# Kernel optimization log

Measured on AMD Instinct MI355X. Metric: run time of the kernel, lower is better.

## Reference

```python
import jax, jax.numpy as jnp
import numpy as np
import math

B, N, D = 4, 2048, 512
H, DH = 8, 128
INNER = H * DH


def setup_inputs() -> dict:
    key = jax.random.key(0)
    k1, k2, k3, k4 = jax.random.split(key, 4)
    x = jax.random.normal(k1, (B, N, D), dtype=jnp.float32)
    Wg = jax.random.normal(k2, (D, INNER), dtype=jnp.float32) * (1.0 / math.sqrt(D))
    Wout = jax.random.normal(k3, (INNER, D), dtype=jnp.float32) * (1.0 / math.sqrt(INNER))
    sigma = jax.random.uniform(k4, (1, H, 1, 1), dtype=jnp.float32, minval=0.5, maxval=2.5)
    return {"x": x, "Wg": Wg, "Wout": Wout, "sigma": sigma}


def reference(x, Wg, Wout, sigma):
    b, n, d = x.shape
    h, dh = H, DH
    # value projection: [b,n,d] @ [d, h*dh] -> [b,h,n,dh]
    v = (x @ Wg).reshape(b, n, h, dh).transpose(0, 2, 1, 3)
    # fixed Gaussian positional mask, shared across batch: build once per head
    pos = jnp.arange(1, n + 1, dtype=jnp.float32)
    diffs = jnp.abs(pos[:, None] - pos[None, :])  # [n, n]
    sig = sigma.reshape(h, 1, 1)  # [h,1,1]
    inv_norm = 1.0 / (jnp.sqrt(2.0 * jnp.float32(math.pi)) * sig)
    gauss = inv_norm * jnp.exp(-(diffs[None] ** 2) / (2.0 * sig ** 2))  # [h,n,n]
    corr = gauss / gauss.sum(-1, keepdims=True)  # row-normalized [h,n,n]
    # attention: broadcast mask over batch
    attn = jnp.einsum('hnm,bhmd->bhnd', corr, v)
    out = attn.transpose(0, 2, 1, 3).reshape(b, n, h * dh)
    return out @ Wout  # dropout p=0.0 -> identity
```

## Files before the change

kernel.cpp:

```cpp
#include <hip/hip_runtime.h>
#include <hip/hip_bf16.h>
#include <math.h>

#define B_ 4
#define N_ 2048
#define D_ 512
#define H_ 8
#define DH_ 128
#define INNER_ 1024
#define W_ 32
#define M_ (B_ * N_)

typedef __attribute__((ext_vector_type(8))) short short8;
typedef __attribute__((ext_vector_type(4))) float floatx4;

typedef const __attribute__((address_space(1))) char* gcp;
typedef __attribute__((address_space(3))) char* lcp;

__device__ __forceinline__ unsigned f_to_bf16bits(float f) {
    union { float f; unsigned u; } c; c.f = f;
    return (c.u + 0x7fffu + ((c.u >> 16) & 1u)) >> 16;
}
__device__ __forceinline__ float bf16s_to_f(unsigned short s) {
    union { unsigned u; float f; } c; c.u = ((unsigned)s) << 16; return c.f;
}

#define VST 136

__global__ __launch_bounds__(256, 4) void g1_blur(
    const __hip_bfloat16* __restrict__ x_bf,
    const __hip_bfloat16* __restrict__ Wg_t,
    const float* __restrict__ sigma,
    const float* __restrict__ winv_g,
    __hip_bfloat16* __restrict__ attn)
{
    __shared__ char smem[35328];
    __hip_bfloat16* Asm = (__hip_bfloat16*)smem;
    __hip_bfloat16* Bsm = (__hip_bfloat16*)(smem + 16384);

    const int tid  = threadIdx.x;
    const int lane = tid & 63;
    const int w    = tid >> 6;
    const int wm   = w >> 1;
    const int wn   = w & 1;
    const int quad = lane >> 4;
    const int cl   = lane & 15;

    const int L    = blockIdx.x + 128 * blockIdx.y;
    const int xcd  = L & 7;
    const int idx  = L >> 3;
    const int bm   = xcd * 16 + (idx & 15);
    const int h    = idx >> 4;
    const int n0   = bm * 64;
    const int nb0  = n0 & (N_ - 1);

    floatx4 acc[4][4];
    #pragma unroll
    for (int i = 0; i < 4; ++i)
        #pragma unroll
        for (int j = 0; j < 4; ++j) acc[i][j] = (floatx4){0.f, 0.f, 0.f, 0.f};

    const char* Ab = (const char*)x_bf;
    const char* Bb = (const char*)(Wg_t + (size_t)(h * DH_) * D_);

    for (int k0 = 0; k0 < D_; k0 += 64) {
        #pragma unroll
        for (int it = 0; it < 4; ++it) {
            int o = it * 4096 + tid * 16;
            int r = o >> 7;
            int s = (o >> 4) & 7;
            int c = s ^ (r & 7);
            int gr = n0 - W_ + r;
            gr = gr < 0 ? 0 : (gr > M_ - 1 ? M_ - 1 : gr);
            __builtin_amdgcn_global_load_lds(
                (gcp)(Ab + (size_t)gr * 1024 + k0 * 2 + c * 16), (lcp)(smem + o), 16, 0, 0);
            __builtin_amdgcn_global_load_lds(
                (gcp)(Bb + (size_t)r * 1024 + k0 * 2 + c * 16), (lcp)(smem + 16384 + o), 16, 0, 0);
        }
        __syncthreads();

        const short* As = (const short*)Asm;
        const short* Bs = (const short*)Bsm;
        #pragma unroll
        for (int kk = 0; kk < 2; ++kk) {
            short8 af[4], bf[4];
            int ch = kk * 4 + quad;
            #pragma unroll
            for (int t = 0; t < 4; ++t) {
                int ra = wm * 64 + t * 16 + cl;
                int rb = wn * 64 + t * 16 + cl;
                af[t] = *(const short8*)(As + ra * 64 + ((ch ^ (ra & 7)) * 8));
                bf[t] = *(const short8*)(Bs + rb * 64 + ((ch ^ (rb & 7)) * 8));
            }
            #pragma unroll
            for (int i = 0; i < 4; ++i)
                #pragma unroll
                for (int j = 0; j < 4; ++j)
                    acc[i][j] = __builtin_amdgcn_mfma_f32_16x16x32_bf16(
                        af[i], bf[j], acc[i][j], 0, 0, 0);
        }
        __syncthreads();
    }

    unsigned short* vsT   = (unsigned short*)smem;
    unsigned short* wtabS = (unsigned short*)(smem + 34816);

    #pragma unroll
    for (int i = 0; i < 4; ++i) {
        #pragma unroll
        for (int j = 0; j < 4; ++j) {
            int ch   = wn * 64 + j * 16 + cl;
            int row0 = wm * 64 + i * 16 + quad * 4;
            unsigned p01 = 0u, p23 = 0u;
            #pragma unroll
            for (int rr = 0; rr < 4; ++rr) {
                int vb = nb0 - W_ + row0 + rr;
                unsigned bits = (vb >= 0 && vb < N_) ? f_to_bf16bits(acc[i][j][rr]) : 0u;
                if (rr < 2) p01 |= bits << (rr * 16);
                else        p23 |= bits << ((rr - 2) * 16);
            }
            unsigned* dst = (unsigned*)(vsT + ch * VST + row0);
            dst[0] = p01; dst[1] = p23;
        }
    }
    if (tid <= 2 * W_) {
        float sig = sigma[h];
        float d = (float)(tid - W_);
        wtabS[tid] = (unsigned short)f_to_bf16bits(__expf(-d * d / (2.0f * sig * sig)));
    }
    __syncthreads();

    short afr[2][3][8];
    #pragma unroll
    for (int mi = 0; mi < 2; ++mi) {
        int row = wm * 32 + mi * 16 + cl;
        #pragma unroll
        for (int t = 0; t < 3; ++t) {
            int lb = (wm + t) * 32 + quad * 8 - row;
            #pragma unroll
            for (int j = 0; j < 8; ++j) {
                int l = lb + j;
                afr[mi][t][j] = (l >= 0 && l <= 2 * W_) ? (short)wtabS[l] : (short)0;
            }
        }
    }

    floatx4 oacc[2][4];
    #pragma unroll
    for (int mi = 0; mi < 2; ++mi)
        #pragma unroll
        for (int ni = 0; ni < 4; ++ni) oacc[mi][ni] = (floatx4){0.f, 0.f, 0.f, 0.f};

    #pragma unroll
    for (int t = 0; t < 3; ++t) {
        int k4 = wm + t;
        short8 bfr[4];
        #pragma unroll
        for (int ni = 0; ni < 4; ++ni) {
            int ch = wn * 64 + ni * 16 + cl;
            bfr[ni] = *(const short8*)((const short*)vsT + ch * VST + k4 * 32 + quad * 8);
        }
        #pragma unroll
        for (int mi = 0; mi < 2; ++mi)
            #pragma unroll
            for (int ni = 0; ni < 4; ++ni)
                oacc[mi][ni] = __builtin_amdgcn_mfma_f32_16x16x32_bf16(
                    *(short8*)afr[mi][t], bfr[ni], oacc[mi][ni], 0, 0, 0);
    }

    float wv[2][4];
    #pragma unroll
    for (int mi = 0; mi < 2; ++mi)
        #pragma unroll
        for (int r = 0; r < 4; ++r)
            wv[mi][r] = winv_g[h * N_ + nb0 + wm * 32 + mi * 16 + quad * 4 + r];

    #pragma unroll
    for (int mi = 0; mi < 2; ++mi) {
        #pragma unroll
        for (int ni = 0; ni < 4; ++ni) {
            int ch = wn * 64 + ni * 16 + cl;
            #pragma unroll
            for (int r = 0; r < 4; ++r) {
                int orow = wm * 32 + mi * 16 + quad * 4 + r;
                attn[(size_t)(n0 + orow) * INNER_ + h * DH_ + ch] =
                    __float2bfloat16(oacc[mi][ni][r] * wv[mi][r]);
            }
        }
    }
}

__global__ __launch_bounds__(256, 3) void gemm2_dbuf(
    const __hip_bfloat16* __restrict__ A,
    const __hip_bfloat16* __restrict__ Bt,
    float* __restrict__ C)
{
    __shared__ char smem[49152];

    const int bid  = blockIdx.x;
    const int xcd  = bid & 7;
    const int idx  = bid >> 3;
    const int bm   = xcd * 16 + (idx & 15);
    const int bn   = idx >> 4;

    const int tid  = threadIdx.x;
    const int lane = tid & 63;
    const int w    = tid >> 6;
    const int wm   = w >> 1;
    const int wn   = w & 1;
    const int kh   = lane >> 4;
    const int ml   = lane & 15;

    floatx4 acc[2][4];
    #pragma unroll
    for (int i = 0; i < 2; ++i)
        #pragma unroll
        for (int j = 0; j < 4; ++j) acc[i][j] = (floatx4){0.f, 0.f, 0.f, 0.f};

    const char* Ab = (const char*)(A + (size_t)(bm * 64) * INNER_);
    const char* Bb = (const char*)(Bt + (size_t)(bn * 128) * INNER_);

    auto issue = [&](int buf, int k0) {
        #pragma unroll
        for (int it = 0; it < 2; ++it) {
            int o = it * 4096 + tid * 16;
            int r = o >> 7;
            int c = ((o >> 4) & 7) ^ (r & 7);
            __builtin_amdgcn_global_load_lds(
                (gcp)(Ab + (size_t)r * 2048 + k0 * 2 + c * 16),
                (lcp)(smem + buf * 24576 + o), 16, 0, 0);
        }
        #pragma unroll
        for (int it = 0; it < 4; ++it) {
            int o = it * 4096 + tid * 16;
            int r = o >> 7;
            int c = ((o >> 4) & 7) ^ (r & 7);
            __builtin_amdgcn_global_load_lds(
                (gcp)(Bb + (size_t)r * 2048 + k0 * 2 + c * 16),
                (lcp)(smem + buf * 24576 + 8192 + o), 16, 0, 0);
        }
    };
    auto consume = [&](int buf) {
        const short* As = (const short*)(smem + buf * 24576);
        const short* Bs = (const short*)(smem + buf * 24576 + 8192);
        short8 af[2][2], bf[4][2];
        #pragma unroll
        for (int t = 0; t < 2; ++t) {
            int ra = wm * 32 + t * 16 + ml;
            #pragma unroll
            for (int kk = 0; kk < 2; ++kk) {
                int ch = kk * 4 + kh;
                af[t][kk] = *(const short8*)(As + ra * 64 + ((ch ^ (ra & 7)) * 8));
            }
        }
        #pragma unroll
        for (int ni = 0; ni < 4; ++ni) {
            int rb = wn * 64 + ni * 16 + ml;
            #pragma unroll
            for (int kk = 0; kk < 2; ++kk) {
                int ch = kk * 4 + kh;
                bf[ni][kk] = *(const short8*)(Bs + rb * 64 + ((ch ^ (rb & 7)) * 8));
            }
        }
        #pragma unroll
        for (int kk = 0; kk < 2; ++kk)
            #pragma unroll
            for (int i = 0; i < 2; ++i)
                #pragma unroll
                for (int j = 0; j < 4; ++j)
                    acc[i][j] = __builtin_amdgcn_mfma_f32_16x16x32_bf16(
                        af[i][kk], bf[j][kk], acc[i][j], 0, 0, 0);
    };

    const int nk = INNER_ >> 6;
    issue(0, 0);
    for (int kt = 0; kt < nk; kt += 2) {
        __syncthreads();
        if (kt + 1 < nk) issue(1, (kt + 1) << 6);
        consume(0);
        __syncthreads();
        if (kt + 2 < nk) issue(0, (kt + 2) << 6);
        consume(1);
    }
    __syncthreads();

    float* Cs = (float*)smem;
    const int rq = lane >> 4;
    const int cl = lane & 15;
    #pragma unroll
    for (int i = 0; i < 2; ++i)
        #pragma unroll
        for (int j = 0; j < 4; ++j)
            #pragma unroll
            for (int r = 0; r < 4; ++r)
                Cs[(wm * 32 + i * 16 + rq * 4 + r) * 128 + wn * 64 + j * 16 + cl] = acc[i][j][r];
    __syncthreads();

    #pragma unroll
    for (int p = 0; p < 8; ++p) {
        int idx2 = p * 256 + tid;
        int rr = idx2 >> 5;
        int cc = (idx2 & 31) * 4;
        float4 vv = *(const float4*)(Cs + rr * 128 + cc);
        *(float4*)(C + (size_t)(bm * 64 + rr) * D_ + bn * 128 + cc) = vv;
    }
}

__device__ __forceinline__ void transpose32(
    const float* __restrict__ src, __hip_bfloat16* __restrict__ dst,
    int R, int Cn, int rt, int ct, int tid)
{
    __shared__ float t[32][33];
    int c0 = ct * 32, r0 = rt * 32;
    int lx = tid & 31, ly = tid >> 5;
    #pragma unroll
    for (int i = 0; i < 32; i += 8)
        t[ly + i][lx] = src[(size_t)(r0 + ly + i) * Cn + c0 + lx];
    __syncthreads();
    #pragma unroll
    for (int i = 0; i < 32; i += 8)
        dst[(size_t)(c0 + ly + i) * R + r0 + lx] = __float2bfloat16(t[lx][ly + i]);
}

__global__ __launch_bounds__(256) void prep(
    const float* __restrict__ x, const float* __restrict__ Wg,
    const float* __restrict__ Wout, const float* __restrict__ sigma,
    __hip_bfloat16* __restrict__ x_bf, __hip_bfloat16* __restrict__ Wg_t,
    __hip_bfloat16* __restrict__ Wout_t, float* __restrict__ winv_g)
{
    const int bid = blockIdx.x;
    const int tid = threadIdx.x;
    if (bid < 2048) {
        int i = bid * 256 + tid;
        const float4* s = (const float4*)x + (size_t)i * 2;
        float4 a = s[0], b = s[1];
        __hip_bfloat16 o[8] = {
            __float2bfloat16(a.x), __float2bfloat16(a.y), __float2bfloat16(a.z), __float2bfloat16(a.w),
            __float2bfloat16(b.x), __float2bfloat16(b.y), __float2bfloat16(b.z), __float2bfloat16(b.w)};
        *(short8*)(x_bf + (size_t)i * 8) = *(short8*)o;
    } else if (bid < 2560) {
        int id2 = bid - 2048;
        transpose32(Wg, Wg_t, D_, INNER_, id2 >> 5, id2 & 31, tid);
    } else if (bid < 3072) {
        int id2 = bid - 2560;
        transpose32(Wout, Wout_t, INNER_, D_, id2 >> 4, id2 & 15, tid);
    } else {
        int idx = (bid - 3072) * 256 + tid;
        int hh = idx >> 11;
        int n  = idx & (N_ - 1);
        float sig = sigma[hh];
        float ws = 0.f;
        for (int l = 0; l <= 2 * W_; ++l) {
            int vb = n + l - W_;
            if (vb >= 0 && vb < N_) {
                float d = (float)(l - W_);
                ws += bf16s_to_f((unsigned short)f_to_bf16bits(
                    __expf(-d * d / (2.0f * sig * sig))));
            }
        }
        winv_g[idx] = 1.0f / ws;
    }
}

extern "C" void kernel_launch(void* const* d_in, const int* in_sizes, int n_in,
                              void* d_out, int out_size, void* d_ws, size_t ws_size,
                              hipStream_t stream) {
    const float* x     = (const float*)d_in[0];
    const float* Wg    = (const float*)d_in[1];
    const float* Wout  = (const float*)d_in[2];
    const float* sigma = (const float*)d_in[3];
    float* out = (float*)d_out;

    char* ws = (char*)d_ws;
    __hip_bfloat16* x_bf   = (__hip_bfloat16*)ws;
    __hip_bfloat16* Wg_t   = (__hip_bfloat16*)(ws + (((size_t)8)  << 20));
    __hip_bfloat16* Wout_t = (__hip_bfloat16*)(ws + (((size_t)9)  << 20));
    __hip_bfloat16* attn   = (__hip_bfloat16*)(ws + (((size_t)10) << 20));
    float*          winv_g = (float*)(ws + (((size_t)26) << 20));

    prep<<<dim3(3136), dim3(256), 0, stream>>>(x, Wg, Wout, sigma,
                                               x_bf, Wg_t, Wout_t, winv_g);

    g1_blur<<<dim3(M_ / 64, H_), dim3(256), 0, stream>>>(x_bf, Wg_t, sigma, winv_g, attn);

    gemm2_dbuf<<<dim3(512), dim3(256), 0, stream>>>(attn, Wout_t, out);
}
```

Before: 118.4 us.

## Enlarge fused projection-blur tile to 128 rows to cut halo recompute

The fused value-projection plus Gaussian blur kernel now covers 128 output rows per block instead of 64, using 512 threads and a 192-row projection tile. This lowers the share of redundant halo rows recomputed in the first GEMM from 2x to 1.5x. The cost is more LDS and fewer, larger blocks (512 in total), which reduces occupancy and wave-level parallelism. The load of the normalization weights is also hoisted ahead of the blur stage.

```diff
diff --git a/kernel.cpp b/kernel.cpp
--- a/kernel.cpp
+++ b/kernel.cpp
@@ -25,18 +25,18 @@
     union { unsigned u; float f; } c; c.u = ((unsigned)s) << 16; return c.f;
 }
 
-#define VST 136
-
-__global__ __launch_bounds__(256, 4) void g1_blur(
+#define VST2 200
+#define AROWS 192
+#define BOFF 24576
+
+__global__ __launch_bounds__(512, 2) void g1_blur(
     const __hip_bfloat16* __restrict__ x_bf,
     const __hip_bfloat16* __restrict__ Wg_t,
     const float* __restrict__ sigma,
     const float* __restrict__ winv_g,
     __hip_bfloat16* __restrict__ attn)
 {
-    __shared__ char smem[35328];
-    __hip_bfloat16* Asm = (__hip_bfloat16*)smem;
-    __hip_bfloat16* Bsm = (__hip_bfloat16*)(smem + 16384);
+    __shared__ char smem[51456];
 
     const int tid  = threadIdx.x;
     const int lane = tid & 63;
@@ -46,17 +46,17 @@
     const int quad = lane >> 4;
     const int cl   = lane & 15;
 
-    const int L    = blockIdx.x + 128 * blockIdx.y;
+    const int L    = blockIdx.x + 64 * blockIdx.y;
     const int xcd  = L & 7;
     const int idx  = L >> 3;
-    const int bm   = xcd * 16 + (idx & 15);
-    const int h    = idx >> 4;
-    const int n0   = bm * 64;
+    const int bm   = xcd * 8 + (idx & 7);
+    const int h    = idx >> 3;
+    const int n0   = bm * 128;
     const int nb0  = n0 & (N_ - 1);
 
-    floatx4 acc[4][4];
-    #pragma unroll
-    for (int i = 0; i < 4; ++i)
+    floatx4 acc[3][4];
+    #pragma unroll
+    for (int i = 0; i < 3; ++i)
         #pragma unroll
         for (int j = 0; j < 4; ++j) acc[i][j] = (floatx4){0.f, 0.f, 0.f, 0.f};
 
@@ -65,35 +65,43 @@
 
     for (int k0 = 0; k0 < D_; k0 += 64) {
         #pragma unroll
-        for (int it = 0; it < 4; ++it) {
-            int o = it * 4096 + tid * 16;
+        for (int it = 0; it < 3; ++it) {
+            int o = it * 8192 + tid * 16;
             int r = o >> 7;
-            int s = (o >> 4) & 7;
-            int c = s ^ (r & 7);
+            int c = ((o >> 4) & 7) ^ (r & 7);
             int gr = n0 - W_ + r;
             gr = gr < 0 ? 0 : (gr > M_ - 1 ? M_ - 1 : gr);
             __builtin_amdgcn_global_load_lds(
                 (gcp)(Ab + (size_t)gr * 1024 + k0 * 2 + c * 16), (lcp)(smem + o), 16, 0, 0);
+        }
+        #pragma unroll
+        for (int it = 0; it < 2; ++it) {
+            int o = it * 8192 + tid * 16;
+            int r = o >> 7;
+            int c = ((o >> 4) & 7) ^ (r & 7);
             __builtin_amdgcn_global_load_lds(
-                (gcp)(Bb + (size_t)r * 1024 + k0 * 2 + c * 16), (lcp)(smem + 16384 + o), 16, 0, 0);
+                (gcp)(Bb + (size_t)r * 1024 + k0 * 2 + c * 16), (lcp)(smem + BOFF + o), 16, 0, 0);
         }
         __syncthreads();
 
-        const short* As = (const short*)Asm;
-        const short* Bs = (const short*)Bsm;
+        const short* As = (const short*)smem;
+        const short* Bs = (const short*)(smem + BOFF);
         #pragma unroll
         for (int kk = 0; kk < 2; ++kk) {
-            short8 af[4], bf[4];
+            short8 af[3], bf[4];
             int ch = kk * 4 + quad;
             #pragma unroll
+            for (int t = 0; t < 3; ++t) {
+                int ra = wm * 48 + t * 16 + cl;
+                af[t] = *(const short8*)(As + ra * 64 + ((ch ^ (ra & 7)) * 8));
+            }
+            #pragma unroll
             for (int t = 0; t < 4; ++t) {
-                int ra = wm * 64 + t * 16 + cl;
                 int rb = wn * 64 + t * 16 + cl;
-                af[t] = *(const short8*)(As + ra * 64 + ((ch ^ (ra & 7)) * 8));
                 bf[t] = *(const short8*)(Bs + rb * 64 + ((ch ^ (rb & 7)) * 8));
             }
             #pragma unroll
-            for (int i = 0; i < 4; ++i)
+            for (int i = 0; i < 3; ++i)
                 #pragma unroll
                 for (int j = 0; j < 4; ++j)
                     acc[i][j] = __builtin_amdgcn_mfma_f32_16x16x32_bf16(
@@ -102,15 +110,22 @@
         __syncthreads();
     }
 
+    float wv[2][4];
+    #pragma unroll
+    for (int mi = 0; mi < 2; ++mi)
+        #pragma unroll
+        for (int r = 0; r < 4; ++r)
+            wv[mi][r] = winv_g[h * N_ + nb0 + wm * 32 + mi * 16 + quad * 4 + r];
+
     unsigned short* vsT   = (unsigned short*)smem;
-    unsigned short* wtabS = (unsigned short*)(smem + 34816);
-
-    #pragma unroll
-    for (int i = 0; i < 4; ++i) {
+    unsigned short* wtabS = (unsigned short*)(smem + 51200);
+
+    #pragma unroll
+    for (int i = 0; i < 3; ++i) {
         #pragma unroll
         for (int j = 0; j < 4; ++j) {
             int ch   = wn * 64 + j * 16 + cl;
-            int row0 = wm * 64 + i * 16 + quad * 4;
+            int row0 = wm * 48 + i * 16 + quad * 4;
             unsigned p01 = 0u, p23 = 0u;
             #pragma unroll
             for (int rr = 0; rr < 4; ++rr) {
@@ -119,7 +134,7 @@
                 if (rr < 2) p01 |= bits << (rr * 16);
                 else        p23 |= bits << ((rr - 2) * 16);
             }
-            unsigned* dst = (unsigned*)(vsT + ch * VST + row0);
+            unsigned* dst = (unsigned*)(vsT + ch * VST2 + row0);
             dst[0] = p01; dst[1] = p23;
         }
     }
@@ -153,12 +168,12 @@
 
     #pragma unroll
     for (int t = 0; t < 3; ++t) {
-        int k4 = wm + t;
+        int k32 = wm + t;
         short8 bfr[4];
         #pragma unroll
         for (int ni = 0; ni < 4; ++ni) {
             int ch = wn * 64 + ni * 16 + cl;
-            bfr[ni] = *(const short8*)((const short*)vsT + ch * VST + k4 * 32 + quad * 8);
+            bfr[ni] = *(const short8*)((const short*)vsT + ch * VST2 + k32 * 32 + quad * 8);
         }
         #pragma unroll
         for (int mi = 0; mi < 2; ++mi)
@@ -167,13 +182,6 @@
                 oacc[mi][ni] = __builtin_amdgcn_mfma_f32_16x16x32_bf16(
                     *(short8*)afr[mi][t], bfr[ni], oacc[mi][ni], 0, 0, 0);
     }
-
-    float wv[2][4];
-    #pragma unroll
-    for (int mi = 0; mi < 2; ++mi)
-        #pragma unroll
-        for (int r = 0; r < 4; ++r)
-            wv[mi][r] = winv_g[h * N_ + nb0 + wm * 32 + mi * 16 + quad * 4 + r];
 
     #pragma unroll
     for (int mi = 0; mi < 2; ++mi) {
@@ -381,7 +389,7 @@
     prep<<<dim3(3136), dim3(256), 0, stream>>>(x, Wg, Wout, sigma,
                                                x_bf, Wg_t, Wout_t, winv_g);
 
-    g1_blur<<<dim3(M_ / 64, H_), dim3(256), 0, stream>>>(x_bf, Wg_t, sigma, winv_g, attn);
+    g1_blur<<<dim3(64, H_), dim3(512), 0, stream>>>(x_bf, Wg_t, sigma, winv_g, attn);
 
     gemm2_dbuf<<<dim3(512), dim3(256), 0, stream>>>(attn, Wout_t, out);
 }
```

After: 112.1 us. -5.3%, faster.
